# Performance work log

Hardware: AMD Instinct MI355X
Metric: run time of the kernel (lower is better)

The kernel has to match this reference:

```python
import math
import jax, jax.numpy as jnp
import numpy as np

B, N, D, H = 8, 512, 1024, 16
HD = D // H
K_DEFAULT, K_MAX, PROX_THR = 8, 12, 20.0


def setup_inputs() -> dict:
    key = jax.random.key(0)
    ks = jax.random.split(key, 12)
    tokens_B = jax.random.normal(ks[0], (B, N, D), dtype=jnp.float32)
    ego_distances = jax.random.uniform(ks[1], (B, N), dtype=jnp.float32)
    ego_mask = jnp.zeros((B, N), dtype=bool).at[:, 0].set(True)  # token 0 is ego
    ego_speed = jax.random.uniform(ks[2], (B,), dtype=jnp.float32)
    s = 1.0 / math.sqrt(D)
    Wq = jax.random.normal(ks[3], (D, D), jnp.float32) * s
    Wk = jax.random.normal(ks[4], (D, D), jnp.float32) * s
    Wv = jax.random.normal(ks[5], (D, D), jnp.float32) * s
    Weq = jax.random.normal(ks[6], (D, D), jnp.float32) * s
    Wo = jax.random.normal(ks[7], (D, D), jnp.float32) * (0.02 * s)
    Dm = D // 4
    W1 = jax.random.normal(ks[8], (Dm, 2), jnp.float32) * (1.0 / math.sqrt(2))
    b1 = jnp.zeros((Dm,), jnp.float32)
    W2 = jax.random.normal(ks[9], (H, Dm), jnp.float32) * (1.0 / math.sqrt(Dm))
    b2 = jnp.zeros((H,), jnp.float32)
    return dict(tokens_B=tokens_B, ego_distances=ego_distances, ego_mask=ego_mask,
                ego_speed=ego_speed, Wq=Wq, Wk=Wk, Wv=Wv, Weq=Weq, Wo=Wo,
                W1=W1, b1=b1, W2=W2, b2=b2)


def _compute_K(ego_speed, ego_distances):
    # deterministic, no-grad lookup (torch: @torch.no_grad)
    n = ego_distances.shape[1]
    close = (ego_distances < PROX_THR).astype(jnp.float32).sum(-1)
    density = close / max(n, 1)
    avg_speed = float(jnp.mean(ego_speed))
    avg_density = float(jnp.mean(density))
    K = K_DEFAULT
    if avg_speed > 15.0:
        K = min(K + 1, K_MAX)
    if avg_density > 0.5:
        K = min(K + 1, K_MAX)
    return min(K, n - 1)


def reference(tokens_B, ego_distances, ego_mask, ego_speed, Wq, Wk, Wv, Weq, Wo, W1, b1, W2, b2):
    b, n, d = tokens_B.shape
    K = _compute_K(ego_speed, ego_distances)
    if K <= 0:
        return jnp.zeros_like(tokens_B)

    # top-K nearest-to-ego neighbors per token, excluding self
    eye = jnp.eye(n, dtype=bool)
    dist_rank = jnp.where(eye[None, :, :], jnp.inf, ego_distances[:, None, :])  # (B,N,N)
    _, topk_idx = jax.lax.top_k(-dist_rank, K)  # (B,N,K) indices of smallest dists

    neighbors = jax.vmap(lambda t, idx: t[idx])(tokens_B, topk_idx)  # (B,N,K,D)

    is_ego = ego_mask.astype(tokens_B.dtype)[..., None]
    Q = (1.0 - is_ego) * (tokens_B @ Wq.T) + is_ego * (tokens_B @ Weq.T)
    Km = neighbors @ Wk.T
    Vm = neighbors @ Wv.T

    Q = Q.reshape(b, n, H, HD).transpose(0, 2, 1, 3)              # (B,H,N,hd)
    Km = Km.reshape(b, n, K, H, HD).transpose(0, 3, 1, 2, 4)      # (B,H,N,K,hd)
    Vm = Vm.reshape(b, n, K, H, HD).transpose(0, 3, 1, 2, 4)

    scores = jnp.einsum('bhnd,bhnkd->bhnk', Q, Km) / math.sqrt(HD)

    # additive pairwise distance bias MLP on (d_i_to_ego, d_j_to_ego)
    d_i = jnp.broadcast_to(ego_distances[:, :, None], (b, n, K))
    d_j = jax.vmap(lambda dd, idx: dd[idx])(ego_distances, topk_idx)
    dist_pair = jnp.stack([d_i, d_j], axis=-1)                    # (B,N,K,2)
    bias = jax.nn.relu(dist_pair @ W1.T + b1) @ W2.T + b2         # (B,N,K,H)
    scores = scores + bias.transpose(0, 3, 1, 2)                  # FIX-1: additive

    attn = jax.nn.softmax(scores, axis=-1)
    out = jnp.einsum('bhnk,bhnkd->bhnd', attn, Vm)
    out = out.transpose(0, 2, 1, 3).reshape(b, n, d)              # FIX-2 axis order
    return out @ Wo.T
```

## Files before the change

### kernel.cpp

```cpp
#include <hip/hip_runtime.h>
#include <math.h>

#define Bn 8
#define Nn 512
#define Dn 1024
#define Hn 16
#define HDn 64
#define KMAX 12
#define NSMAX 13
#define PROX 20.0f

typedef __attribute__((ext_vector_type(8))) short bf16x8;
typedef __attribute__((ext_vector_type(4))) float f32x4;

__device__ __forceinline__ unsigned short f2bf(float f) {
    unsigned int u = __float_as_uint(f);
    return (unsigned short)((u + 0x7FFFu + ((u >> 16) & 1u)) >> 16);
}

__global__ __launch_bounds__(256) void cvt_meta_kernel(const float* __restrict__ tokens,
                                                       const float* __restrict__ Wq,
                                                       const float* __restrict__ Wo,
                                                       const float* __restrict__ Wk,
                                                       const float* __restrict__ Wv,
                                                       const float* __restrict__ dist,
                                                       const float* __restrict__ speed,
                                                       unsigned short* __restrict__ tok_h,
                                                       unsigned short* __restrict__ wq_h,
                                                       unsigned short* __restrict__ wo_h,
                                                       unsigned short* __restrict__ wkv_h,
                                                       int* __restrict__ meta,
                                                       int* __restrict__ Lidx,
                                                       unsigned short* __restrict__ tok_g) {
    int blk = blockIdx.x;
    if (blk < 8192) {
        const float* src;
        unsigned short* dst;
        int local;
        if (blk < 4096) { src = tokens; dst = tok_h; local = blk; }
        else if (blk < 5120) { src = Wq; dst = wq_h; local = blk - 4096; }
        else if (blk < 6144) { src = Wo; dst = wo_h; local = blk - 5120; }
        else if (blk < 7168) { src = Wk; dst = wkv_h; local = blk - 6144; }
        else { src = Wv; dst = wkv_h + (size_t)Dn * Dn; local = blk - 7168; }
        int i = (local * 256 + threadIdx.x) * 4;
        float4 v = *(const float4*)&src[i];
        ushort4 o;
        o.x = f2bf(v.x); o.y = f2bf(v.y); o.z = f2bf(v.z); o.w = f2bf(v.w);
        *(ushort4*)&dst[i] = o;
        return;
    }
    if (threadIdx.x >= 64) return;
    int lane = threadIdx.x;
    int b = blk - 8192;

    int cnt = 0;
    for (int i = lane; i < Bn * Nn; i += 64) cnt += (dist[i] < PROX) ? 1 : 0;
    for (int off = 32; off; off >>= 1) cnt += __shfl_xor(cnt, off);

    float sp = 0.f;
    for (int i = lane; i < Bn; i += 64) sp += speed[i];
    for (int off = 32; off; off >>= 1) sp += __shfl_xor(sp, off);

    float avg_density = (float)cnt / (float)(Bn * Nn);
    float avg_speed = sp / (float)Bn;
    int K = 8;
    if (avg_speed > 15.0f) K = min(K + 1, KMAX);
    if (avg_density > 0.5f) K = min(K + 1, KMAX);
    K = min(K, Nn - 1);
    if (b == 0 && lane == 0) meta[0] = K;
    int ns = K + 1;

    int sel[NSMAX];
    float dloc[Nn / 64];
    #pragma unroll
    for (int j = 0; j < Nn / 64; ++j) dloc[j] = dist[b * Nn + lane + 64 * j];
    for (int r = 0; r < ns; ++r) {
        float mv = 1e30f;
        int mi = 0;
        #pragma unroll
        for (int j = 0; j < Nn / 64; ++j) {
            if (dloc[j] < mv) { mv = dloc[j]; mi = lane + 64 * j; }
        }
        for (int off = 32; off; off >>= 1) {
            float ov = __shfl_xor(mv, off);
            int oi = __shfl_xor(mi, off);
            if (ov < mv || (ov == mv && oi < mi)) { mv = ov; mi = oi; }
        }
        sel[r] = mi;
        if (lane == 0) Lidx[b * NSMAX + r] = mi;
        if ((mi & 63) == lane) dloc[mi >> 6] = 1e30f;
    }

    for (int s = 0; s < ns; ++s) {
        const float* src = &tokens[(size_t)(b * Nn + sel[s]) * Dn];
        unsigned short* dst = &tok_g[(size_t)(b * 16 + s) * Dn];
        #pragma unroll
        for (int q = 0; q < 4; ++q) {
            float4 v = *(const float4*)&src[(q * 64 + lane) * 4];
            ushort4 o;
            o.x = f2bf(v.x); o.y = f2bf(v.y); o.z = f2bf(v.z); o.w = f2bf(v.w);
            *(ushort4*)&dst[(q * 64 + lane) * 4] = o;
        }
    }
}

__device__ __forceinline__ void gemm_body_s(const unsigned short* A,
                                            const unsigned short* Bm,
                                            float* Cf, unsigned short* Ch,
                                            int Nd, int Kd, int sA, int sB,
                                            int bm, int bn, int mode, int hh,
                                            unsigned short* As, unsigned short* Bs) {
    int t = threadIdx.x;
    int wave = t >> 6, lane = t & 63;
    int wm = wave >> 1, wn = wave & 1;

    int srow = lane >> 2;
    int skoff = (lane & 3) * 8;
    const unsigned short* Ag  = A  + (size_t)(bm + wave * 16 + srow) * sA + skoff;
    const unsigned short* Bg  = Bm + (size_t)(bn + wave * 32 + srow) * sB + skoff;
    const unsigned short* Bg2 = Bg + (size_t)16 * sB;

    f32x4 acc[2][4] = {};
    int fm = lane & 15;
    int fk = (lane >> 4) * 8;

    auto stage = [&](int buf) {
        unsigned short* AsW  = As + buf * 2048 + (wave * 16) * 32;
        unsigned short* BsW  = Bs + buf * 4096 + (wave * 32) * 32;
        __builtin_amdgcn_global_load_lds((const __attribute__((address_space(1))) void*)Ag,
                                         (__attribute__((address_space(3))) void*)AsW, 16, 0, 0);
        __builtin_amdgcn_global_load_lds((const __attribute__((address_space(1))) void*)Bg,
                                         (__attribute__((address_space(3))) void*)BsW, 16, 0, 0);
        __builtin_amdgcn_global_load_lds((const __attribute__((address_space(1))) void*)Bg2,
                                         (__attribute__((address_space(3))) void*)(BsW + 512), 16, 0, 0);
        Ag += 32; Bg += 32; Bg2 += 32;
    };

    int nsteps = Kd >> 5;
    stage(0);
    __syncthreads();
    int cur = 0;
    for (int s = 0; s < nsteps; ++s) {
        if (s + 1 < nsteps) stage(cur ^ 1);
        const unsigned short* Ab = As + cur * 2048;
        const unsigned short* Bb = Bs + cur * 4096;
        bf16x8 af[2], bfr[4];
        #pragma unroll
        for (int mi = 0; mi < 2; ++mi)
            af[mi] = *(const bf16x8*)&Ab[(wm * 32 + mi * 16 + fm) * 32 + fk];
        #pragma unroll
        for (int ni = 0; ni < 4; ++ni)
            bfr[ni] = *(const bf16x8*)&Bb[(wn * 64 + ni * 16 + fm) * 32 + fk];
        #pragma unroll
        for (int mi = 0; mi < 2; ++mi)
            #pragma unroll
            for (int ni = 0; ni < 4; ++ni)
                acc[mi][ni] = __builtin_amdgcn_mfma_f32_16x16x32_bf16(af[mi], bfr[ni], acc[mi][ni], 0, 0, 0);
        __syncthreads();
        cur ^= 1;
    }

    int erow = (lane >> 4) * 4;
    #pragma unroll
    for (int mi = 0; mi < 2; ++mi)
        #pragma unroll
        for (int ni = 0; ni < 4; ++ni)
            #pragma unroll
            for (int r = 0; r < 4; ++r) {
                int row = bm + wm * 32 + mi * 16 + erow + r;
                int col = bn + wn * 64 + ni * 16 + fm;
                if (mode == 0) {
                    Cf[(size_t)row * Nd + col] = acc[mi][ni][r];
                } else if (mode == 1) {
                    Ch[(size_t)row * Nd + col] = f2bf(acc[mi][ni][r]);
                } else {
                    int bb = col >> 4, ss = col & 15;
                    Ch[((size_t)bb * 1024 + row) * 256 + ss * 16 + hh] = f2bf(acc[mi][ni][r]);
                }
            }
}

__global__ __launch_bounds__(256) void proj_fused_kernel(const unsigned short* __restrict__ tok_h,
                                                         const unsigned short* __restrict__ wq_h,
                                                         const unsigned short* __restrict__ tok_g,
                                                         const unsigned short* __restrict__ wkv_h,
                                                         const float* __restrict__ tokens,
                                                         const float* __restrict__ Weq,
                                                         float* __restrict__ Qbuf,
                                                         float* __restrict__ Kproj,
                                                         unsigned short* __restrict__ v_h,
                                                         float* __restrict__ Qego) {
    __shared__ unsigned short As[2 * 64 * 32];
    __shared__ unsigned short Bs[2 * 128 * 32];
    __shared__ float tok[Dn];

    int blk = blockIdx.x;
    if (blk < 16) {
        gemm_body_s(tok_g, wkv_h, Kproj, 0, Dn, Dn, Dn, Dn,
                    (blk >> 3) * 64, (blk & 7) * 128, 0, 0, As, Bs);
    } else if (blk < 32) {
        int idx = blk - 16;
        gemm_body_s(tok_g, wkv_h + (size_t)Dn * Dn, 0, v_h, Dn, Dn, Dn, Dn,
                    (idx >> 3) * 64, (idx & 7) * 128, 1, 0, As, Bs);
    } else if (blk < 544) {
        int idx = blk - 32;
        gemm_body_s(tok_h, wq_h, Qbuf, 0, Dn, Dn, Dn, Dn,
                    (idx >> 3) * 64, (idx & 7) * 128, 0, 0, As, Bs);
    } else {
        int blk2 = blk - 544;
        int b = blk2 >> 5, cg = blk2 & 31;
        for (int t = threadIdx.x; t < Dn; t += 256) tok[t] = tokens[(size_t)(b * Nn) * Dn + t];
        __syncthreads();
        int w = threadIdx.x >> 6, lane = threadIdx.x & 63;
        for (int o = 0; o < 8; ++o) {
            int col = cg * 32 + w * 8 + o;
            const float* wr = &Weq[(size_t)col * Dn];
            float sum = 0.f;
            #pragma unroll
            for (int q = 0; q < 4; ++q) {
                float4 w4 = *(const float4*)&wr[q * 256 + lane * 4];
                float4 t4 = *(const float4*)&tok[q * 256 + lane * 4];
                sum += w4.x * t4.x + w4.y * t4.y + w4.z * t4.z + w4.w * t4.w;
            }
            for (int off = 32; off; off >>= 1) sum += __shfl_xor(sum, off);
            if (lane == 0) Qego[(size_t)b * Dn + col] = sum;
        }
    }
}

__global__ __launch_bounds__(256) void vo3_gemm_kernel(const unsigned short* __restrict__ wo_h,
                                                       const unsigned short* __restrict__ v_h,
                                                       unsigned short* __restrict__ Vo3T) {
    __shared__ unsigned short As[2 * 64 * 32];
    __shared__ unsigned short Bs[2 * 128 * 32];
    int h = blockIdx.y;
    gemm_body_s(wo_h + h * HDn, v_h + h * HDn, 0, Vo3T, 0, HDn, Dn, Dn,
                blockIdx.x * 64, 0, 2, h, As, Bs);
}

#define HSTR 264
__global__ __launch_bounds__(256) void attn_kernel(const float* __restrict__ Q,
                                                   const float* __restrict__ Qego,
                                                   const float* __restrict__ Kproj,
                                                   const float* __restrict__ dist,
                                                   const float* __restrict__ W1,
                                                   const float* __restrict__ b1,
                                                   const float* __restrict__ W2,
                                                   const float* __restrict__ b2,
                                                   const int* __restrict__ meta,
                                                   const int* __restrict__ Lidx,
                                                   unsigned short* __restrict__ Wt) {
    __shared__ float q[Dn];
    __shared__ float hid[KMAX * HSTR];
    __shared__ float sc[Hn * NSMAX];
    __shared__ float at[Hn * NSMAX];
    __shared__ int selslot[NSMAX];
    __shared__ int inv[16];
    __shared__ float dj[NSMAX];

    int bi = blockIdx.x;
    int b = bi >> 9;
    int i = bi & (Nn - 1);
    int K = meta[0];
    int ns = K + 1;
    int t = threadIdx.x;

    float d_i = dist[b * Nn + i];

    if (t < 64) {
        int s = t;
        int jj = (s < ns) ? Lidx[b * NSMAX + s] : -1;
        bool valid = (s < ns) && (jj != i);
        unsigned long long mask = __ballot(valid);
        int rank = __popcll(mask & ((1ull << s) - 1ull));
        bool take = valid && (rank < K);
        if (take) {
            selslot[rank] = s;
            dj[rank] = dist[b * Nn + jj];
        }
        if (s < 16) inv[s] = take ? rank : -1;
    }
    {
        const float* qsrc = (i == 0) ? &Qego[(size_t)b * Dn] : &Q[(size_t)bi * Dn];
        float4 v = *(const float4*)&qsrc[t * 4];
        *(float4*)&q[t * 4] = v;
    }
    __syncthreads();

    {
        float2 w01 = *(const float2*)&W1[2 * t];
        float bb = b1[t];
        for (int k = 0; k < K; ++k) {
            float h = w01.x * d_i + w01.y * dj[k] + bb;
            hid[k * HSTR + t] = h > 0.f ? h : 0.f;
        }
    }
    __syncthreads();

    {
        int g = t >> 4, l = t & 15;
        float4 qv = *(const float4*)&q[g * HDn + l * 4];
        float4 w2v[4];
        #pragma unroll
        for (int ii = 0; ii < 4; ++ii)
            w2v[ii] = *(const float4*)&W2[g * 256 + ii * 64 + l * 4];
        float bias0 = b2[g];

        for (int k = 0; k < K; ++k) {
            int row = b * 16 + selslot[k];
            float4 kv4 = *(const float4*)&Kproj[(size_t)row * Dn + g * HDn + l * 4];
            float val = (qv.x * kv4.x + qv.y * kv4.y + qv.z * kv4.z + qv.w * kv4.w) * 0.125f;
            #pragma unroll
            for (int ii = 0; ii < 4; ++ii) {
                float4 h4 = *(const float4*)&hid[k * HSTR + ii * 64 + l * 4];
                val += w2v[ii].x * h4.x + w2v[ii].y * h4.y + w2v[ii].z * h4.z + w2v[ii].w * h4.w;
            }
            val += __shfl_xor(val, 1);
            val += __shfl_xor(val, 2);
            val += __shfl_xor(val, 4);
            val += __shfl_xor(val, 8);
            if (l == 0) sc[g * NSMAX + k] = val + bias0;
        }
    }
    __syncthreads();

    if (t < Hn) {
        int h = t;
        float m = -1e30f;
        for (int k = 0; k < K; ++k) m = fmaxf(m, sc[h * NSMAX + k]);
        float ssum = 0.f;
        for (int k = 0; k < K; ++k) {
            float e = expf(sc[h * NSMAX + k] - m);
            at[h * NSMAX + k] = e;
            ssum += e;
        }
        float inv2 = 1.f / ssum;
        for (int k = 0; k < K; ++k) at[h * NSMAX + k] *= inv2;
    }
    __syncthreads();

    {
        int s = t >> 4, h = t & 15;
        int k = (s < NSMAX) ? inv[s] : -1;
        float a = (k >= 0) ? at[h * NSMAX + k] : 0.f;
        Wt[(size_t)bi * 256 + t] = f2bf(a);
    }
}

__global__ __launch_bounds__(256) void final_gemm_kernel(const unsigned short* __restrict__ Wt,
                                                         const unsigned short* __restrict__ Vo3T,
                                                         float* __restrict__ out) {
    __shared__ unsigned short As[2 * 64 * 32];
    __shared__ unsigned short Bs[2 * 128 * 32];
    int rbase = blockIdx.y * 64;
    int b = rbase >> 9;
    int bmloc = rbase & (Nn - 1);
    gemm_body_s(Wt + (size_t)b * Nn * 256,
                Vo3T + (size_t)b * Dn * 256,
                out + (size_t)b * Nn * Dn, 0,
                Dn, 256, 256, 256, bmloc, blockIdx.x * 128, 0, 0, As, Bs);
}

extern "C" void kernel_launch(void* const* d_in, const int* in_sizes, int n_in,
                              void* d_out, int out_size, void* d_ws, size_t ws_size,
                              hipStream_t stream) {
    (void)in_sizes; (void)n_in; (void)out_size; (void)ws_size;
    const float* tokens = (const float*)d_in[0];
    const float* dist   = (const float*)d_in[1];
    const float* speed  = (const float*)d_in[3];
    const float* Wq  = (const float*)d_in[4];
    const float* Wk  = (const float*)d_in[5];
    const float* Wv  = (const float*)d_in[6];
    const float* Weq = (const float*)d_in[7];
    const float* Wo  = (const float*)d_in[8];
    const float* W1  = (const float*)d_in[9];
    const float* b1  = (const float*)d_in[10];
    const float* W2  = (const float*)d_in[11];
    const float* b2  = (const float*)d_in[12];
    float* out = (float*)d_out;

    char* ws = (char*)d_ws;
    const size_t SZ_KP   = (size_t)128 * Dn * sizeof(float);
    const size_t SZ_VH   = (size_t)128 * Dn * sizeof(unsigned short);
    const size_t SZ_V3   = (size_t)Bn * Dn * 256 * sizeof(unsigned short);
    const size_t SZ_WT   = (size_t)Bn * Nn * 256 * sizeof(unsigned short);
    const size_t SZ_BIG  = (size_t)Bn * Nn * Dn * sizeof(float);
    const size_t SZ_BIGH = (size_t)Bn * Nn * Dn * sizeof(unsigned short);
    const size_t SZ_WH   = (size_t)Dn * Dn * sizeof(unsigned short);
    const size_t SZ_TG   = (size_t)128 * Dn * sizeof(unsigned short);
    const size_t SZ_QE   = (size_t)Bn * Dn * sizeof(float);

    size_t off = 0;
    int*   meta  = (int*)(ws + off);  off += 256;
    int*   Lidx  = (int*)(ws + off);  off += 768;
    float* Kproj = (float*)(ws + off); off += SZ_KP;
    float* Qbuf  = (float*)(ws + off); off += SZ_BIG;
    float* Qego  = (float*)(ws + off); off += SZ_QE;
    unsigned short* v_h   = (unsigned short*)(ws + off); off += SZ_VH;
    unsigned short* Vo3T  = (unsigned short*)(ws + off); off += SZ_V3;
    unsigned short* Wt    = (unsigned short*)(ws + off); off += SZ_WT;
    unsigned short* tok_h = (unsigned short*)(ws + off); off += SZ_BIGH;
    unsigned short* wq_h  = (unsigned short*)(ws + off); off += SZ_WH;
    unsigned short* wo_h  = (unsigned short*)(ws + off); off += SZ_WH;
    unsigned short* wkv_h = (unsigned short*)(ws + off); off += 2 * SZ_WH;
    unsigned short* tok_g = (unsigned short*)(ws + off); off += SZ_TG;

    cvt_meta_kernel<<<8200, 256, 0, stream>>>(tokens, Wq, Wo, Wk, Wv, dist, speed,
                                              tok_h, wq_h, wo_h, wkv_h, meta, Lidx, tok_g);
    proj_fused_kernel<<<800, 256, 0, stream>>>(tok_h, wq_h, tok_g, wkv_h, tokens, Weq,
                                               Qbuf, Kproj, v_h, Qego);
    vo3_gemm_kernel<<<dim3(16, 16), 256, 0, stream>>>(wo_h, v_h, Vo3T);
    attn_kernel<<<Bn * Nn, 256, 0, stream>>>(Qbuf, Qego, Kproj, dist, W1, b1, W2, b2,
                                             meta, Lidx, Wt);
    final_gemm_kernel<<<dim3(Dn / 128, (Bn * Nn) / 64), 256, 0, stream>>>(Wt, Vo3T, out);
}
```

Before: 179.3 us.

## Replace Q projection with precomputed Wq-folded key matrix and score GEMM

Stops materialising the full Q = tokens·Wq projection (4096x1024 fp32). Instead it folds Wq into the per-batch candidate keys, building P = Kproj_h·Wq for the 16 candidate slots and all heads, then computes every query-candidate score with one GEMM of tokens against P. The attention kernel now reads precomputed scores, and only the ego token still uses the explicit Qego dot product. This removes a large GEMM and its fp32 write and read traffic, at the cost of a transposed bf16 Wq, extra bf16 rounding of the keys, and one more kernel launch.

```diff
diff --git a/kernel.cpp b/kernel.cpp
--- a/kernel.cpp
+++ b/kernel.cpp
@@ -26,32 +26,63 @@
                                                        const float* __restrict__ dist,
                                                        const float* __restrict__ speed,
                                                        unsigned short* __restrict__ tok_h,
-                                                       unsigned short* __restrict__ wq_h,
+                                                       unsigned short* __restrict__ wqT,
                                                        unsigned short* __restrict__ wo_h,
                                                        unsigned short* __restrict__ wkv_h,
                                                        int* __restrict__ meta,
                                                        int* __restrict__ Lidx,
                                                        unsigned short* __restrict__ tok_g) {
+    __shared__ unsigned short tl[64][72];
     int blk = blockIdx.x;
-    if (blk < 8192) {
+    int t = threadIdx.x;
+
+    if (blk >= 4096 && blk < 4352) {
+        int tb = blk - 4096;
+        int tr = tb >> 4, tc = tb & 15;
+        #pragma unroll
+        for (int it = 0; it < 4; ++it) {
+            int lin = it * 256 + t;
+            int row = lin >> 4;
+            int c4  = lin & 15;
+            float4 v = *(const float4*)&Wq[(size_t)(tr * 64 + row) * Dn + tc * 64 + c4 * 4];
+            tl[c4 * 4 + 0][row] = f2bf(v.x);
+            tl[c4 * 4 + 1][row] = f2bf(v.y);
+            tl[c4 * 4 + 2][row] = f2bf(v.z);
+            tl[c4 * 4 + 3][row] = f2bf(v.w);
+        }
+        __syncthreads();
+        #pragma unroll
+        for (int it = 0; it < 4; ++it) {
+            int lin = it * 256 + t;
+            int cc = lin >> 4;
+            int d4 = lin & 15;
+            ushort4 o;
+            o.x = tl[cc][d4 * 4 + 0];
+            o.y = tl[cc][d4 * 4 + 1];
+            o.z = tl[cc][d4 * 4 + 2];
+            o.w = tl[cc][d4 * 4 + 3];
+            *(ushort4*)&wqT[(size_t)(tc * 64 + cc) * Dn + tr * 64 + d4 * 4] = o;
+        }
+        return;
+    }
+    if (blk < 7424) {
         const float* src;
         unsigned short* dst;
         int local;
         if (blk < 4096) { src = tokens; dst = tok_h; local = blk; }
-        else if (blk < 5120) { src = Wq; dst = wq_h; local = blk - 4096; }
-        else if (blk < 6144) { src = Wo; dst = wo_h; local = blk - 5120; }
-        else if (blk < 7168) { src = Wk; dst = wkv_h; local = blk - 6144; }
-        else { src = Wv; dst = wkv_h + (size_t)Dn * Dn; local = blk - 7168; }
-        int i = (local * 256 + threadIdx.x) * 4;
+        else if (blk < 5376) { src = Wo; dst = wo_h; local = blk - 4352; }
+        else if (blk < 6400) { src = Wk; dst = wkv_h; local = blk - 5376; }
+        else { src = Wv; dst = wkv_h + (size_t)Dn * Dn; local = blk - 6400; }
+        int i = (local * 256 + t) * 4;
         float4 v = *(const float4*)&src[i];
         ushort4 o;
         o.x = f2bf(v.x); o.y = f2bf(v.y); o.z = f2bf(v.z); o.w = f2bf(v.w);
         *(ushort4*)&dst[i] = o;
         return;
     }
-    if (threadIdx.x >= 64) return;
-    int lane = threadIdx.x;
-    int b = blk - 8192;
+    if (t >= 64) return;
+    int lane = t;
+    int b = blk - 7424;
 
     int cnt = 0;
     for (int i = lane; i < Bn * Nn; i += 64) cnt += (dist[i] < PROX) ? 1 : 0;
@@ -169,25 +200,29 @@
             for (int r = 0; r < 4; ++r) {
                 int row = bm + wm * 32 + mi * 16 + erow + r;
                 int col = bn + wn * 64 + ni * 16 + fm;
+                float v = acc[mi][ni][r];
                 if (mode == 0) {
-                    Cf[(size_t)row * Nd + col] = acc[mi][ni][r];
+                    Cf[(size_t)row * Nd + col] = v;
                 } else if (mode == 1) {
-                    Ch[(size_t)row * Nd + col] = f2bf(acc[mi][ni][r]);
+                    Ch[(size_t)row * Nd + col] = f2bf(v);
+                } else if (mode == 2) {
+                    int bb = col >> 4, ss = col & 15;
+                    Ch[((size_t)bb * 1024 + row) * 256 + ss * 16 + hh] = f2bf(v);
+                } else if (mode == 3) {
+                    Ch[(((size_t)(row >> 4) << 8) + ((row & 15) << 4) + hh) * 1024 + col] = f2bf(v);
                 } else {
-                    int bb = col >> 4, ss = col & 15;
-                    Ch[((size_t)bb * 1024 + row) * 256 + ss * 16 + hh] = f2bf(acc[mi][ni][r]);
+                    Cf[(size_t)row * Nd + col] = v;
+                    Ch[(size_t)row * Nd + col] = f2bf(v);
                 }
             }
 }
 
-__global__ __launch_bounds__(256) void proj_fused_kernel(const unsigned short* __restrict__ tok_h,
-                                                         const unsigned short* __restrict__ wq_h,
-                                                         const unsigned short* __restrict__ tok_g,
+__global__ __launch_bounds__(256) void proj_fused_kernel(const unsigned short* __restrict__ tok_g,
                                                          const unsigned short* __restrict__ wkv_h,
                                                          const float* __restrict__ tokens,
                                                          const float* __restrict__ Weq,
-                                                         float* __restrict__ Qbuf,
                                                          float* __restrict__ Kproj,
+                                                         unsigned short* __restrict__ kp_h,
                                                          unsigned short* __restrict__ v_h,
                                                          float* __restrict__ Qego) {
     __shared__ unsigned short As[2 * 64 * 32];
@@ -196,20 +231,16 @@
 
     int blk = blockIdx.x;
     if (blk < 16) {
-        gemm_body_s(tok_g, wkv_h, Kproj, 0, Dn, Dn, Dn, Dn,
-                    (blk >> 3) * 64, (blk & 7) * 128, 0, 0, As, Bs);
+        gemm_body_s(tok_g, wkv_h, Kproj, kp_h, Dn, Dn, Dn, Dn,
+                    (blk >> 3) * 64, (blk & 7) * 128, 4, 0, As, Bs);
     } else if (blk < 32) {
         int idx = blk - 16;
         gemm_body_s(tok_g, wkv_h + (size_t)Dn * Dn, 0, v_h, Dn, Dn, Dn, Dn,
                     (idx >> 3) * 64, (idx & 7) * 128, 1, 0, As, Bs);
-    } else if (blk < 544) {
-        int idx = blk - 32;
-        gemm_body_s(tok_h, wq_h, Qbuf, 0, Dn, Dn, Dn, Dn,
-                    (idx >> 3) * 64, (idx & 7) * 128, 0, 0, As, Bs);
     } else {
-        int blk2 = blk - 544;
+        int blk2 = blk - 32;
         int b = blk2 >> 5, cg = blk2 & 31;
-        for (int t = threadIdx.x; t < Dn; t += 256) tok[t] = tokens[(size_t)(b * Nn) * Dn + t];
+        for (int tt = threadIdx.x; tt < Dn; tt += 256) tok[tt] = tokens[(size_t)(b * Nn) * Dn + tt];
         __syncthreads();
         int w = threadIdx.x >> 6, lane = threadIdx.x & 63;
         for (int o = 0; o < 8; ++o) {
@@ -228,29 +259,56 @@
     }
 }
 
-__global__ __launch_bounds__(256) void vo3_gemm_kernel(const unsigned short* __restrict__ wo_h,
-                                                       const unsigned short* __restrict__ v_h,
-                                                       unsigned short* __restrict__ Vo3T) {
+__global__ __launch_bounds__(256) void pbuild_vo3_kernel(const unsigned short* __restrict__ kp_h,
+                                                         const unsigned short* __restrict__ wqT,
+                                                         unsigned short* __restrict__ P,
+                                                         const unsigned short* __restrict__ wo_h,
+                                                         const unsigned short* __restrict__ v_h,
+                                                         unsigned short* __restrict__ Vo3T) {
     __shared__ unsigned short As[2 * 64 * 32];
     __shared__ unsigned short Bs[2 * 128 * 32];
-    int h = blockIdx.y;
-    gemm_body_s(wo_h + h * HDn, v_h + h * HDn, 0, Vo3T, 0, HDn, Dn, Dn,
-                blockIdx.x * 64, 0, 2, h, As, Bs);
+    int blk = blockIdx.x;
+    if (blk < 256) {
+        int h = blk >> 4;
+        int rt = (blk >> 3) & 1, ct = blk & 7;
+        gemm_body_s(kp_h + h * HDn, wqT + h * HDn, 0, P, 0, HDn, Dn, Dn,
+                    rt * 64, ct * 128, 3, h, As, Bs);
+    } else {
+        int v = blk - 256;
+        int h = v >> 4, rt = v & 15;
+        gemm_body_s(wo_h + h * HDn, v_h + h * HDn, 0, Vo3T, 0, HDn, Dn, Dn,
+                    rt * 64, 0, 2, h, As, Bs);
+    }
+}
+
+__global__ __launch_bounds__(256) void scores_gemm_kernel(const unsigned short* __restrict__ tok_h,
+                                                          const unsigned short* __restrict__ P,
+                                                          float* __restrict__ scores) {
+    __shared__ unsigned short As[2 * 64 * 32];
+    __shared__ unsigned short Bs[2 * 128 * 32];
+    int idx = blockIdx.x;
+    int b = idx >> 4;
+    int rt = (idx >> 1) & 7, ct = idx & 1;
+    gemm_body_s(tok_h + (size_t)b * Nn * Dn,
+                P + (size_t)b * 256 * Dn,
+                scores + (size_t)b * Nn * 256, 0,
+                256, Dn, Dn, Dn, rt * 64, ct * 128, 0, 0, As, Bs);
 }
 
 #define HSTR 264
-__global__ __launch_bounds__(256) void attn_kernel(const float* __restrict__ Q,
-                                                   const float* __restrict__ Qego,
-                                                   const float* __restrict__ Kproj,
-                                                   const float* __restrict__ dist,
-                                                   const float* __restrict__ W1,
-                                                   const float* __restrict__ b1,
-                                                   const float* __restrict__ W2,
-                                                   const float* __restrict__ b2,
-                                                   const int* __restrict__ meta,
-                                                   const int* __restrict__ Lidx,
-                                                   unsigned short* __restrict__ Wt) {
+__global__ __launch_bounds__(256) void attn_lite_kernel(const float* __restrict__ scores,
+                                                        const float* __restrict__ Qego,
+                                                        const float* __restrict__ Kproj,
+                                                        const float* __restrict__ dist,
+                                                        const float* __restrict__ W1,
+                                                        const float* __restrict__ b1,
+                                                        const float* __restrict__ W2,
+                                                        const float* __restrict__ b2,
+                                                        const int* __restrict__ meta,
+                                                        const int* __restrict__ Lidx,
+                                                        unsigned short* __restrict__ Wt) {
     __shared__ float q[Dn];
+    __shared__ float scq[256];
     __shared__ float hid[KMAX * HSTR];
     __shared__ float sc[Hn * NSMAX];
     __shared__ float at[Hn * NSMAX];
@@ -280,9 +338,9 @@
         }
         if (s < 16) inv[s] = take ? rank : -1;
     }
-    {
-        const float* qsrc = (i == 0) ? &Qego[(size_t)b * Dn] : &Q[(size_t)bi * Dn];
-        float4 v = *(const float4*)&qsrc[t * 4];
+    scq[t] = scores[(size_t)bi * 256 + t];
+    if (i == 0) {
+        float4 v = *(const float4*)&Qego[(size_t)b * Dn + t * 4];
         *(float4*)&q[t * 4] = v;
     }
     __syncthreads();
@@ -299,7 +357,8 @@
 
     {
         int g = t >> 4, l = t & 15;
-        float4 qv = *(const float4*)&q[g * HDn + l * 4];
+        float4 qv = {0.f, 0.f, 0.f, 0.f};
+        if (i == 0) qv = *(const float4*)&q[g * HDn + l * 4];
         float4 w2v[4];
         #pragma unroll
         for (int ii = 0; ii < 4; ++ii)
@@ -307,9 +366,15 @@
         float bias0 = b2[g];
 
         for (int k = 0; k < K; ++k) {
-            int row = b * 16 + selslot[k];
-            float4 kv4 = *(const float4*)&Kproj[(size_t)row * Dn + g * HDn + l * 4];
-            float val = (qv.x * kv4.x + qv.y * kv4.y + qv.z * kv4.z + qv.w * kv4.w) * 0.125f;
+            int slot = selslot[k];
+            float val;
+            if (i == 0) {
+                int row = b * 16 + slot;
+                float4 kv4 = *(const float4*)&Kproj[(size_t)row * Dn + g * HDn + l * 4];
+                val = (qv.x * kv4.x + qv.y * kv4.y + qv.z * kv4.z + qv.w * kv4.w) * 0.125f;
+            } else {
+                val = (l == 0) ? scq[slot * 16 + g] * 0.125f : 0.f;
+            }
             #pragma unroll
             for (int ii = 0; ii < 4; ++ii) {
                 float4 h4 = *(const float4*)&hid[k * HSTR + ii * 64 + l * 4];
@@ -381,10 +446,12 @@
 
     char* ws = (char*)d_ws;
     const size_t SZ_KP   = (size_t)128 * Dn * sizeof(float);
+    const size_t SZ_KPH  = (size_t)128 * Dn * sizeof(unsigned short);
     const size_t SZ_VH   = (size_t)128 * Dn * sizeof(unsigned short);
     const size_t SZ_V3   = (size_t)Bn * Dn * 256 * sizeof(unsigned short);
     const size_t SZ_WT   = (size_t)Bn * Nn * 256 * sizeof(unsigned short);
-    const size_t SZ_BIG  = (size_t)Bn * Nn * Dn * sizeof(float);
+    const size_t SZ_SC   = (size_t)Bn * Nn * 256 * sizeof(float);
+    const size_t SZ_P    = (size_t)Bn * 256 * Dn * sizeof(unsigned short);
     const size_t SZ_BIGH = (size_t)Bn * Nn * Dn * sizeof(unsigned short);
     const size_t SZ_WH   = (size_t)Dn * Dn * sizeof(unsigned short);
     const size_t SZ_TG   = (size_t)128 * Dn * sizeof(unsigned short);
@@ -394,23 +461,26 @@
     int*   meta  = (int*)(ws + off);  off += 256;
     int*   Lidx  = (int*)(ws + off);  off += 768;
     float* Kproj = (float*)(ws + off); off += SZ_KP;
-    float* Qbuf  = (float*)(ws + off); off += SZ_BIG;
+    float* scores= (float*)(ws + off); off += SZ_SC;
     float* Qego  = (float*)(ws + off); off += SZ_QE;
+    unsigned short* kp_h  = (unsigned short*)(ws + off); off += SZ_KPH;
+    unsigned short* P     = (unsigned short*)(ws + off); off += SZ_P;
     unsigned short* v_h   = (unsigned short*)(ws + off); off += SZ_VH;
     unsigned short* Vo3T  = (unsigned short*)(ws + off); off += SZ_V3;
     unsigned short* Wt    = (unsigned short*)(ws + off); off += SZ_WT;
     unsigned short* tok_h = (unsigned short*)(ws + off); off += SZ_BIGH;
-    unsigned short* wq_h  = (unsigned short*)(ws + off); off += SZ_WH;
+    unsigned short* wqT   = (unsigned short*)(ws + off); off += SZ_WH;
     unsigned short* wo_h  = (unsigned short*)(ws + off); off += SZ_WH;
     unsigned short* wkv_h = (unsigned short*)(ws + off); off += 2 * SZ_WH;
     unsigned short* tok_g = (unsigned short*)(ws + off); off += SZ_TG;
 
-    cvt_meta_kernel<<<8200, 256, 0, stream>>>(tokens, Wq, Wo, Wk, Wv, dist, speed,
-                                              tok_h, wq_h, wo_h, wkv_h, meta, Lidx, tok_g);
-    proj_fused_kernel<<<800, 256, 0, stream>>>(tok_h, wq_h, tok_g, wkv_h, tokens, Weq,
-                                               Qbuf, Kproj, v_h, Qego);
-    vo3_gemm_kernel<<<dim3(16, 16), 256, 0, stream>>>(wo_h, v_h, Vo3T);
-    attn_kernel<<<Bn * Nn, 256, 0, stream>>>(Qbuf, Qego, Kproj, dist, W1, b1, W2, b2,
-                                             meta, Lidx, Wt);
+    cvt_meta_kernel<<<7432, 256, 0, stream>>>(tokens, Wq, Wo, Wk, Wv, dist, speed,
+                                              tok_h, wqT, wo_h, wkv_h, meta, Lidx, tok_g);
+    proj_fused_kernel<<<288, 256, 0, stream>>>(tok_g, wkv_h, tokens, Weq,
+                                               Kproj, kp_h, v_h, Qego);
+    pbuild_vo3_kernel<<<512, 256, 0, stream>>>(kp_h, wqT, P, wo_h, v_h, Vo3T);
+    scores_gemm_kernel<<<128, 256, 0, stream>>>(tok_h, P, scores);
+    attn_lite_kernel<<<Bn * Nn, 256, 0, stream>>>(scores, Qego, Kproj, dist, W1, b1, W2, b2,
+                                                  meta, Lidx, Wt);
     final_gemm_kernel<<<dim3(Dn / 128, (Bn * Nn) / 64), 256, 0, stream>>>(Wt, Vo3T, out);
 }
```

After: 191.9 us. 1.07x slower.
